# Kernel optimization log

Measured on AMD Instinct MI355X. Metric: run time of the kernel, lower is better.

The kernel has to match this reference:

```python
import jax, jax.numpy as jnp
import numpy as np

N_STATE = 1024
N_HEAD = 16
HEAD_DIM = N_STATE // N_HEAD


def setup_inputs() -> dict:
    key = jax.random.key(0)
    ks = jax.random.split(key, 8)
    s = 0.02
    return {
        "x": jax.random.normal(ks[0], (4, 1500, N_STATE), dtype=jnp.float32),
        "Wq": jax.random.normal(ks[1], (N_STATE, N_STATE), dtype=jnp.float32) * s,
        "bq": jnp.zeros((N_STATE,), dtype=jnp.float32),
        "Wk": jax.random.normal(ks[2], (N_STATE, N_STATE), dtype=jnp.float32) * s,
        "Wv": jax.random.normal(ks[3], (N_STATE, N_STATE), dtype=jnp.float32) * s,
        "bv": jnp.zeros((N_STATE,), dtype=jnp.float32),
        "Wo": jax.random.normal(ks[4], (N_STATE, N_STATE), dtype=jnp.float32) * s,
        "bo": jnp.zeros((N_STATE,), dtype=jnp.float32),
    }


def reference(x, Wq, bq, Wk, Wv, bv, Wo, bo):
    B, S, _ = x.shape
    scale = HEAD_DIM ** (-0.5)
    # projections (torch Linear: y = x @ W.T + b)
    q = x @ Wq.T + bq
    k = x @ Wk.T
    v = x @ Wv.T + bv
    # [B, H, S, D]
    q = q.reshape(B, S, N_HEAD, HEAD_DIM).transpose(0, 2, 1, 3)
    k = k.reshape(B, S, N_HEAD, HEAD_DIM).transpose(0, 2, 1, 3)
    v = v.reshape(B, S, N_HEAD, HEAD_DIM).transpose(0, 2, 1, 3)
    # scores scaled AFTER the matmul, as in the original (qk * qk_scale)
    qk = jnp.einsum("bhqd,bhkd->bhqk", q, k) * scale
    w = jax.nn.softmax(qk, axis=-1)
    wv = jnp.einsum("bhqk,bhkd->bhqd", w, v)
    wv = wv.transpose(0, 2, 1, 3).reshape(B, S, N_STATE)
    return wv @ Wo.T + bo
```

## Files before the change

### kernel.cpp

```cpp
#include <hip/hip_runtime.h>
#include <stdint.h>

#define S_LEN  1500
#define S_PAD  1536
#define BATCH  4
#define NSTATE 1024
#define NHEAD  16
#define HDIM   64
#define MROWS  6000
#define C1 0.180336879f

typedef __attribute__((ext_vector_type(8)))  short short8;
typedef __attribute__((ext_vector_type(4)))  float floatx4;
typedef __attribute__((ext_vector_type(16))) float floatx16;

__device__ __forceinline__ unsigned short f2bf(float f) {
  union { float f; unsigned int u; } v; v.f = f;
  unsigned int r = v.u + 0x7fffu + ((v.u >> 16) & 1u);
  return (unsigned short)(r >> 16);
}

__device__ __forceinline__ void gld_lds16(const void* g, void* l) {
  __builtin_amdgcn_global_load_lds(
      (const __attribute__((address_space(1))) void*)g,
      (__attribute__((address_space(3))) void*)l, 16, 0, 0);
}

__global__ __launch_bounds__(256) void cvt_all(
    const float* __restrict__ x,  const float* __restrict__ Wq,
    const float* __restrict__ Wk, const float* __restrict__ Wv,
    const float* __restrict__ Wo, unsigned short* __restrict__ dst,
    unsigned short* __restrict__ vt)
{
  const size_t NX   = (size_t)MROWS * NSTATE;
  const size_t NTOT = NX + 4u * 1024u * 1024u;
  size_t e = ((size_t)blockIdx.x * 256 + threadIdx.x) * 4;
  if (e >= NTOT) {
    size_t p = (e - NTOT) >> 2;
    int row = (int)(p / 9);
    int off = (int)(p % 9) * 4;
    uint2 z; z.x = 0u; z.y = 0u;
    *(uint2*)&vt[(size_t)row * S_PAD + 1500 + off] = z;
    return;
  }
  const float* src; size_t off;
  if (e < NX) { src = x; off = e; }
  else {
    size_t t = e - NX;
    int wsel = (int)(t >> 20);
    off = t & ((1u << 20) - 1);
    src = (wsel == 0) ? Wq : (wsel == 1) ? Wk : (wsel == 2) ? Wv : Wo;
  }
  float4 v = *(const float4*)(src + off);
  uint2 o;
  o.x = (unsigned int)f2bf(v.x) | ((unsigned int)f2bf(v.y) << 16);
  o.y = (unsigned int)f2bf(v.z) | ((unsigned int)f2bf(v.w) << 16);
  *(uint2*)(dst + e) = o;
}

__device__ __forceinline__ void gemm128_32(
    const unsigned short* __restrict__ X,
    const unsigned short* __restrict__ W,
    const float* __restrict__ bias,
    void* __restrict__ Yv,
    int m0, int n0, float oscale, int outmode)
{
  __shared__ unsigned short As[2][128 * 32];
  __shared__ unsigned short Bs[2][128 * 32];

  const int tid  = threadIdx.x;
  const int lane = tid & 63;
  const int wid  = tid >> 6;
  const int wm   = (wid & 1) * 64;
  const int wn   = (wid >> 1) * 64;
  const int l31  = lane & 31;
  const int lhi  = lane >> 5;
  const int fr   = (l31 >> 1) & 3;

  floatx16 acc[2][2];
#pragma unroll
  for (int i = 0; i < 2; ++i)
#pragma unroll
    for (int j = 0; j < 2; ++j)
      acc[i][j] = (floatx16)(0.f);

  const int srow = tid >> 2;
  const int logc = (lane & 3) ^ ((srow >> 1) & 3);

  const char* xrp[2];
  const char* wrp[2];
#pragma unroll
  for (int r = 0; r < 2; ++r) {
    int arow = m0 + r * 64 + srow;
    if (arow > MROWS - 1) arow = MROWS - 1;
    xrp[r] = (const char*)X + (size_t)arow * NSTATE * 2 + logc * 16;
    int brow = n0 + r * 64 + srow;
    wrp[r] = (const char*)W + (size_t)brow * NSTATE * 2 + logc * 16;
  }

  auto stage = [&](int t, int bi) {
    const int kb = t * 64;
    gld_lds16(xrp[0] + kb, (char*)As[bi] + 0 * 4096 + wid * 1024);
    gld_lds16(xrp[1] + kb, (char*)As[bi] + 1 * 4096 + wid * 1024);
    gld_lds16(wrp[0] + kb, (char*)Bs[bi] + 0 * 4096 + wid * 1024);
    gld_lds16(wrp[1] + kb, (char*)Bs[bi] + 1 * 4096 + wid * 1024);
  };

  stage(0, 0);
  __syncthreads();

  for (int t = 0; t < 32; ++t) {
    const int cur = t & 1;
    if (t < 31) stage(t + 1, cur ^ 1);

    short8 af[2][2], bf[2][2];
#pragma unroll
    for (int mt = 0; mt < 2; ++mt)
#pragma unroll
      for (int kc = 0; kc < 2; ++kc) {
        int row  = wm + mt * 32 + l31;
        int phys = (kc * 2 + lhi) ^ fr;
        af[mt][kc] = *(const short8*)(As[cur] + row * 32 + phys * 8);
      }
#pragma unroll
    for (int nt = 0; nt < 2; ++nt)
#pragma unroll
      for (int kc = 0; kc < 2; ++kc) {
        int row  = wn + nt * 32 + l31;
        int phys = (kc * 2 + lhi) ^ fr;
        bf[nt][kc] = *(const short8*)(Bs[cur] + row * 32 + phys * 8);
      }
    __builtin_amdgcn_s_setprio(1);
#pragma unroll
    for (int mt = 0; mt < 2; ++mt)
#pragma unroll
      for (int nt = 0; nt < 2; ++nt)
#pragma unroll
        for (int kc = 0; kc < 2; ++kc)
          acc[mt][nt] = __builtin_amdgcn_mfma_f32_32x32x16_bf16(
              af[mt][kc], bf[nt][kc], acc[mt][nt], 0, 0, 0);
    __builtin_amdgcn_s_setprio(0);

    __syncthreads();
  }

  if (outmode == 2) {
    unsigned short* vt = (unsigned short*)Yv;
#pragma unroll
    for (int nt = 0; nt < 2; ++nt) {
      int ng = n0 + wn + nt * 32 + l31;
      float bias_v = bias[ng];
      int d  = ng & 63;
      int hh = ng >> 6;
#pragma unroll
      for (int mt = 0; mt < 2; ++mt)
#pragma unroll
        for (int rq = 0; rq < 4; ++rq) {
          int mgq = m0 + wm + mt * 32 + 8 * rq + 4 * lhi;
          if (mgq < MROWS) {
            int bb = mgq / 1500;
            int s0 = mgq - 1500 * bb;
            float v0 = acc[mt][nt][rq * 4 + 0] + bias_v;
            float v1 = acc[mt][nt][rq * 4 + 1] + bias_v;
            float v2 = acc[mt][nt][rq * 4 + 2] + bias_v;
            float v3 = acc[mt][nt][rq * 4 + 3] + bias_v;
            uint2 pk2;
            pk2.x = (unsigned int)f2bf(v0) | ((unsigned int)f2bf(v1) << 16);
            pk2.y = (unsigned int)f2bf(v2) | ((unsigned int)f2bf(v3) << 16);
            *(uint2*)&vt[(((size_t)bb * NHEAD + hh) * HDIM + d) * S_PAD + s0] = pk2;
          }
        }
    }
  } else {
#pragma unroll
    for (int nt = 0; nt < 2; ++nt) {
      int ng = n0 + wn + nt * 32 + l31;
      float bias_v = bias ? bias[ng] : 0.f;
#pragma unroll
      for (int mt = 0; mt < 2; ++mt)
#pragma unroll
        for (int r = 0; r < 16; ++r) {
          int mg = m0 + wm + mt * 32 + (r & 3) + 8 * (r >> 2) + 4 * lhi;
          if (mg < MROWS) {
            float val = (acc[mt][nt][r] + bias_v) * oscale;
            if (outmode == 1) ((float*)Yv)[(size_t)mg * NSTATE + ng] = val;
            else ((unsigned short*)Yv)[(size_t)mg * NSTATE + ng] = f2bf(val);
          }
        }
    }
  }
}

__global__ __launch_bounds__(256) void proj_qkv(
    const unsigned short* __restrict__ X,
    const unsigned short* __restrict__ Wq, const unsigned short* __restrict__ Wk,
    const unsigned short* __restrict__ Wv,
    const float* __restrict__ bq, const float* __restrict__ bv,
    unsigned short* __restrict__ q, unsigned short* __restrict__ k,
    unsigned short* __restrict__ vt)
{
  const int id  = blockIdx.x;
  const int sid = (id & 7) * 141 + (id >> 3);
  const int z   = sid / 376;
  const int rem = sid - z * 376;
  const int m0  = (rem >> 3) * 128;
  const int n0  = (rem & 7) * 128;

  if (z == 0)      gemm128_32(X, Wq, bq, q,  m0, n0, C1,  0);
  else if (z == 1) gemm128_32(X, Wk, (const float*)nullptr, k, m0, n0, 1.0f, 0);
  else             gemm128_32(X, Wv, bv, vt, m0, n0, 1.0f, 2);
}

__global__ __launch_bounds__(256) void proj_o(
    const unsigned short* __restrict__ X, const unsigned short* __restrict__ W,
    const float* __restrict__ bias, float* __restrict__ Y)
{
  const int id  = blockIdx.x;
  const int sid = (id & 7) * 47 + (id >> 3);
  gemm128_32(X, W, bias, Y, (sid >> 3) * 128, (sid & 7) * 128, 1.0f, 1);
}

#define NHALF 24

__global__ __launch_bounds__(256, 4) void attn32t(
    const unsigned short* __restrict__ Q, const unsigned short* __restrict__ K,
    const unsigned short* __restrict__ VT, unsigned short* __restrict__ O)
{
  __shared__ unsigned short SMEM[16384];
  unsigned short* Os = SMEM;

  const int tid  = threadIdx.x;
  const int lane = tid & 63;
  const int w    = tid >> 6;
  const int l31  = lane & 31;
  const int lhi  = lane >> 5;

  const int id  = blockIdx.x;
  const int sid = (id & 7) * 96 + (id >> 3);
  const int qt  = sid % 12;
  const int hb  = sid / 12;
  const int h   = hb & 15;
  const int b   = hb >> 4;

  const size_t base  = ((size_t)b * S_LEN) * NSTATE + h * HDIM;
  const size_t vbase = (((size_t)b * NHEAD + h) * HDIM) * S_PAD;

  const int srow8 = lane >> 3;
  const int sc3   = lane & 7;
  const int swc   = sc3 ^ srow8;

  const char* kq0 = (const char*)K +
      (base + (size_t)(w * 16 + srow8) * NSTATE + (size_t)swc * 8) * 2;
  const char* kq1 = kq0 + (size_t)8 * NSTATE * 2;
  const char* vq0 = (const char*)VT +
      (vbase + (size_t)(w * 16 + srow8) * S_PAD + (size_t)swc * 8) * 2;
  const char* vq1 = vq0 + (size_t)8 * S_PAD * 2;

  short8 qf[4];
  {
    int qrow = qt * 128 + w * 32 + l31;
    if (qrow > S_LEN - 1) qrow = S_LEN - 1;
    const unsigned short* qp = Q + base + (size_t)qrow * NSTATE;
#pragma unroll
    for (int c = 0; c < 4; ++c)
      qf[c] = *(const short8*)(qp + c * 16 + lhi * 8);
  }

  short8 ones8;
#pragma unroll
  for (int i = 0; i < 8; ++i) ones8[i] = (short)0x3F80;

  floatx16 oacc[2];
  oacc[0] = (floatx16)(0.f);
  oacc[1] = (floatx16)(0.f);
  floatx16 lacc = (floatx16)(0.f);

  auto stageN = [&](int u, int bi) {
    char* kb = (char*)SMEM + bi * 8192;
    char* vb = (char*)SMEM + 16384 + bi * 8192;
    size_t ko = (size_t)u * (64 * NSTATE * 2);
    size_t vo = (size_t)u * (64 * 2);
    gld_lds16(kq0 + ko, kb + (w * 2 + 0) * 1024);
    gld_lds16(kq1 + ko, kb + (w * 2 + 1) * 1024);
    gld_lds16(vq0 + vo, vb + (w * 2 + 0) * 1024);
    gld_lds16(vq1 + vo, vb + (w * 2 + 1) * 1024);
  };
  auto stageC = [&](int bi) {
    char* kb = (char*)SMEM + bi * 8192;
    char* vb = (char*)SMEM + 16384 + bi * 8192;
#pragma unroll
    for (int qq = 0; qq < 2; ++qq) {
      int s = 1472 + w * 16 + qq * 8 + srow8;
      if (s > S_LEN - 1) s = S_LEN - 1;
      gld_lds16((const char*)K + (base + (size_t)s * NSTATE + (size_t)swc * 8) * 2,
                kb + (w * 2 + qq) * 1024);
    }
    size_t vo = (size_t)23 * (64 * 2);
    gld_lds16(vq0 + vo, vb + (w * 2 + 0) * 1024);
    gld_lds16(vq1 + vo, vb + (w * 2 + 1) * 1024);
  };

  stageN(0, 0);
  __syncthreads();

  for (int u = 0; u < NHALF; ++u) {
    const int cur = u & 1;
    if (u < NHALF - 2)       stageN(u + 1, cur ^ 1);
    else if (u == NHALF - 2) stageC(cur ^ 1);

    const unsigned short* Ks  = SMEM + cur * 4096;
    const unsigned short* Vts = SMEM + 8192 + cur * 4096;

#pragma unroll
    for (int kvt = 0; kvt < 2; ++kvt) {
      int row = kvt * 32 + l31;
      floatx16 sacc = (floatx16)(0.f);
      __builtin_amdgcn_s_setprio(1);
#pragma unroll
      for (int c = 0; c < 4; ++c) {
        int phys = (c * 2 + lhi) ^ (row & 7);
        short8 ak = *(const short8*)(Ks + row * 64 + phys * 8);
        sacc = __builtin_amdgcn_mfma_f32_32x32x16_bf16(ak, qf[c], sacc, 0, 0, 0);
      }
      __builtin_amdgcn_s_setprio(0);

      if (u == NHALF - 1) {
        if (kvt == 1) {
#pragma unroll
          for (int r = 0; r < 16; ++r) sacc[r] = -3.0e38f;
        } else {
#pragma unroll
          for (int r = 12; r < 16; ++r) sacc[r] = lhi ? -3.0e38f : sacc[r];
        }
      }

      unsigned int pk[8];
#pragma unroll
      for (int i = 0; i < 8; ++i) {
        float plo = exp2f(sacc[2 * i]);
        float phi = exp2f(sacc[2 * i + 1]);
        unsigned int rr;
        asm("v_cvt_pk_bf16_f32 %0, %1, %2" : "=v"(rr) : "v"(plo), "v"(phi));
        pk[i] = rr;
      }

      unsigned int a0 = pk[0], a1 = pk[1], b0 = pk[2], b1 = pk[3];
      asm("v_permlane32_swap_b32 %0, %1" : "+v"(a0), "+v"(b0));
      asm("v_permlane32_swap_b32 %0, %1" : "+v"(a1), "+v"(b1));
      unsigned int c0 = pk[4], c1 = pk[5], d0 = pk[6], d1 = pk[7];
      asm("v_permlane32_swap_b32 %0, %1" : "+v"(c0), "+v"(d0));
      asm("v_permlane32_swap_b32 %0, %1" : "+v"(c1), "+v"(d1));
      int4 f0i, f1i;
      f0i.x = a0; f0i.y = a1; f0i.z = b0; f0i.w = b1;
      f1i.x = c0; f1i.y = c1; f1i.z = d0; f1i.w = d1;
      short8 f0 = *(short8*)&f0i;
      short8 f1 = *(short8*)&f1i;

      __builtin_amdgcn_s_setprio(1);
      lacc = __builtin_amdgcn_mfma_f32_32x32x16_bf16(ones8, f0, lacc, 0, 0, 0);
      lacc = __builtin_amdgcn_mfma_f32_32x32x16_bf16(ones8, f1, lacc, 0, 0, 0);

#pragma unroll
      for (int dt = 0; dt < 2; ++dt) {
        int d = dt * 32 + l31;
        int p0 = ((kvt * 4 + 0) + lhi) ^ (d & 7);
        int p1 = ((kvt * 4 + 2) + lhi) ^ (d & 7);
        short8 av0 = *(const short8*)(Vts + d * 64 + p0 * 8);
        short8 av1 = *(const short8*)(Vts + d * 64 + p1 * 8);
        oacc[dt] = __builtin_amdgcn_mfma_f32_32x32x16_bf16(av0, f0, oacc[dt], 0, 0, 0);
        oacc[dt] = __builtin_amdgcn_mfma_f32_32x32x16_bf16(av1, f1, oacc[dt], 0, 0, 0);
      }
      __builtin_amdgcn_s_setprio(0);
    }

    __syncthreads();
  }

  float inv = 1.f / lacc[0];

  __syncthreads();
#pragma unroll
  for (int dt = 0; dt < 2; ++dt)
#pragma unroll
    for (int g = 0; g < 4; ++g) {
      int d0 = dt * 32 + g * 8 + lhi * 4;
      float v0 = oacc[dt][4 * g + 0] * inv;
      float v1 = oacc[dt][4 * g + 1] * inv;
      float v2 = oacc[dt][4 * g + 2] * inv;
      float v3 = oacc[dt][4 * g + 3] * inv;
      uint2 pk2;
      pk2.x = (unsigned int)f2bf(v0) | ((unsigned int)f2bf(v1) << 16);
      pk2.y = (unsigned int)f2bf(v2) | ((unsigned int)f2bf(v3) << 16);
      *(uint2*)&Os[(w * 32 + l31) * 72 + d0] = pk2;
    }
  __syncthreads();
#pragma unroll
  for (int pass = 0; pass < 4; ++pass) {
    int e = pass * 256 + tid;
    int row = e >> 3, ch = e & 7;
    int s = qt * 128 + row;
    if (s < S_LEN)
      *(uint4*)&O[base + (size_t)s * NSTATE + ch * 8] = *(const uint4*)&Os[row * 72 + ch * 8];
  }
}

extern "C" void kernel_launch(void* const* d_in, const int* in_sizes, int n_in,
                              void* d_out, int out_size, void* d_ws, size_t ws_size,
                              hipStream_t stream) {
  const float* x  = (const float*)d_in[0];
  const float* Wq = (const float*)d_in[1];
  const float* bq = (const float*)d_in[2];
  const float* Wk = (const float*)d_in[3];
  const float* Wv = (const float*)d_in[4];
  const float* bv = (const float*)d_in[5];
  const float* Wo = (const float*)d_in[6];
  const float* bo = (const float*)d_in[7];
  float* out = (float*)d_out;

  const size_t NX  = (size_t)MROWS * NSTATE;
  const size_t NW  = (size_t)NSTATE * NSTATE;

  unsigned short* xb  = (unsigned short*)d_ws;
  unsigned short* Wqb = xb  + NX;
  unsigned short* Wkb = Wqb + NW;
  unsigned short* Wvb = Wkb + NW;
  unsigned short* Wob = Wvb + NW;
  unsigned short* q   = Wob + NW;
  unsigned short* k   = q + NX;
  unsigned short* vt  = k + NX;
  unsigned short* wv  = xb;

  const size_t n4_total = (NX + 4 * NW) / 4;
  const int main_blocks = (int)(n4_total / 256);
  const int pad_blocks  = (BATCH * NHEAD * HDIM * 9) / 256;
  cvt_all<<<dim3(main_blocks + pad_blocks), dim3(256), 0, stream>>>(
      x, Wq, Wk, Wv, Wo, xb, vt);
  proj_qkv<<<dim3(1128), dim3(256), 0, stream>>>(xb, Wqb, Wkb, Wvb, bq, bv, q, k, vt);
  attn32t<<<dim3(768), dim3(256), 0, stream>>>(q, k, vt, wv);
  proj_o<<<dim3(376), dim3(256), 0, stream>>>(wv, Wob, bo, out);
}
```

Measured before the change: 255.4 us.

## Deepen GEMM LDS pipeline to four stages with vmcnt-based waits

```diff
diff --git a/kernel.cpp b/kernel.cpp
--- a/kernel.cpp
+++ b/kernel.cpp
@@ -58,15 +58,14 @@
   *(uint2*)(dst + e) = o;
 }
 
-__device__ __forceinline__ void gemm128_32(
+__device__ __forceinline__ void gemm128_p4(
     const unsigned short* __restrict__ X,
     const unsigned short* __restrict__ W,
     const float* __restrict__ bias,
     void* __restrict__ Yv,
     int m0, int n0, float oscale, int outmode)
 {
-  __shared__ unsigned short As[2][128 * 32];
-  __shared__ unsigned short Bs[2][128 * 32];
+  __shared__ char SM[4 * 16384];
 
   const int tid  = threadIdx.x;
   const int lane = tid & 63;
@@ -98,20 +97,31 @@
     wrp[r] = (const char*)W + (size_t)brow * NSTATE * 2 + logc * 16;
   }
 
-  auto stage = [&](int t, int bi) {
+  auto stage = [&](int t, int si) {
     const int kb = t * 64;
-    gld_lds16(xrp[0] + kb, (char*)As[bi] + 0 * 4096 + wid * 1024);
-    gld_lds16(xrp[1] + kb, (char*)As[bi] + 1 * 4096 + wid * 1024);
-    gld_lds16(wrp[0] + kb, (char*)Bs[bi] + 0 * 4096 + wid * 1024);
-    gld_lds16(wrp[1] + kb, (char*)Bs[bi] + 1 * 4096 + wid * 1024);
+    char* ab = SM + si * 16384;
+    char* bb = ab + 8192;
+    gld_lds16(xrp[0] + kb, ab + 0 * 4096 + wid * 1024);
+    gld_lds16(xrp[1] + kb, ab + 1 * 4096 + wid * 1024);
+    gld_lds16(wrp[0] + kb, bb + 0 * 4096 + wid * 1024);
+    gld_lds16(wrp[1] + kb, bb + 1 * 4096 + wid * 1024);
   };
 
   stage(0, 0);
-  __syncthreads();
+  stage(1, 1);
+  stage(2, 2);
 
   for (int t = 0; t < 32; ++t) {
-    const int cur = t & 1;
-    if (t < 31) stage(t + 1, cur ^ 1);
+    if (t < 30)      asm volatile("s_waitcnt vmcnt(8)" ::: "memory");
+    else if (t == 30) asm volatile("s_waitcnt vmcnt(4)" ::: "memory");
+    else             asm volatile("s_waitcnt vmcnt(0)" ::: "memory");
+    __builtin_amdgcn_s_barrier();
+    __builtin_amdgcn_sched_barrier(0);
+
+    if (t < 29) stage(t + 3, (t + 3) & 3);
+
+    const unsigned short* A = (const unsigned short*)(SM + (t & 3) * 16384);
+    const unsigned short* B = (const unsigned short*)(SM + (t & 3) * 16384 + 8192);
 
     short8 af[2][2], bf[2][2];
 #pragma unroll
@@ -120,7 +130,7 @@
       for (int kc = 0; kc < 2; ++kc) {
         int row  = wm + mt * 32 + l31;
         int phys = (kc * 2 + lhi) ^ fr;
-        af[mt][kc] = *(const short8*)(As[cur] + row * 32 + phys * 8);
+        af[mt][kc] = *(const short8*)(A + row * 32 + phys * 8);
       }
 #pragma unroll
     for (int nt = 0; nt < 2; ++nt)
@@ -128,7 +138,7 @@
       for (int kc = 0; kc < 2; ++kc) {
         int row  = wn + nt * 32 + l31;
         int phys = (kc * 2 + lhi) ^ fr;
-        bf[nt][kc] = *(const short8*)(Bs[cur] + row * 32 + phys * 8);
+        bf[nt][kc] = *(const short8*)(B + row * 32 + phys * 8);
       }
     __builtin_amdgcn_s_setprio(1);
 #pragma unroll
@@ -140,8 +150,6 @@
           acc[mt][nt] = __builtin_amdgcn_mfma_f32_32x32x16_bf16(
               af[mt][kc], bf[nt][kc], acc[mt][nt], 0, 0, 0);
     __builtin_amdgcn_s_setprio(0);
-
-    __syncthreads();
   }
 
   if (outmode == 2) {
@@ -206,9 +214,9 @@
   const int m0  = (rem >> 3) * 128;
   const int n0  = (rem & 7) * 128;
 
-  if (z == 0)      gemm128_32(X, Wq, bq, q,  m0, n0, C1,  0);
-  else if (z == 1) gemm128_32(X, Wk, (const float*)nullptr, k, m0, n0, 1.0f, 0);
-  else             gemm128_32(X, Wv, bv, vt, m0, n0, 1.0f, 2);
+  if (z == 0)      gemm128_p4(X, Wq, bq, q,  m0, n0, C1,  0);
+  else if (z == 1) gemm128_p4(X, Wk, (const float*)nullptr, k, m0, n0, 1.0f, 0);
+  else             gemm128_p4(X, Wv, bv, vt, m0, n0, 1.0f, 2);
 }
 
 __global__ __launch_bounds__(256) void proj_o(
@@ -217,7 +225,7 @@
 {
   const int id  = blockIdx.x;
   const int sid = (id & 7) * 47 + (id >> 3);
-  gemm128_32(X, W, bias, Y, (sid >> 3) * 128, (sid & 7) * 128, 1.0f, 1);
+  gemm128_p4(X, W, bias, Y, (sid >> 3) * 128, (sid & 7) * 128, 1.0f, 1);
 }
 
 #define NHALF 24
```

Result: no change. 252.7 us (-1.1%).
